# Kernel tuning notes

Measured on AMD Instinct MI355X. Metric: run time of the kernel, lower is better.

## Reference

```python
import jax, jax.numpy as jnp
import numpy as np

LAMBDA_TV = 0.01
RHO = 1.0
MAX_ITER = 10
CG_ITER = 10


def _fft2c(x):
    # x: (B, 2, H, W) real/imag stacked -> centered ortho FFT, same layout
    xc = x[:, 0] + 1j * x[:, 1]
    kc = jnp.fft.fftshift(
        jnp.fft.fft2(jnp.fft.ifftshift(xc, axes=(-2, -1)), norm='ortho'),
        axes=(-2, -1))
    return jnp.stack([kc.real, kc.imag], axis=1)


def _ifft2c(x):
    xc = x[:, 0] + 1j * x[:, 1]
    ic = jnp.fft.fftshift(
        jnp.fft.ifft2(jnp.fft.ifftshift(xc, axes=(-2, -1)), norm='ortho'),
        axes=(-2, -1))
    return jnp.stack([ic.real, ic.imag], axis=1)


def _gradient(x):
    # forward differences, zero at the far boundary; cat along channel dim
    dx = jnp.concatenate([x[..., 1:] - x[..., :-1], jnp.zeros_like(x[..., :1])], axis=-1)
    dy = jnp.concatenate([x[..., 1:, :] - x[..., :-1, :], jnp.zeros_like(x[..., :1, :])], axis=-2)
    return jnp.concatenate([dx, dy], axis=1)


def _divergence(p):
    # Faithful to the original: only uses channels 0 and 1 of p -> (B,1,H,W)
    px, py = p[:, 0:1], p[:, 1:2]
    div_x = jnp.concatenate(
        [px[..., 0:1], px[..., 1:-1] - px[..., :-2], -px[..., -2:-1]], axis=-1)
    div_y = jnp.concatenate(
        [py[..., 0:1, :], py[..., 1:-1, :] - py[..., :-2, :], -py[..., -2:-1, :]], axis=-2)
    return div_x + div_y


def soft_threshold(x, t):
    return jnp.sign(x) * jnp.maximum(jnp.abs(x) - t, 0.0)


def _cg_solve(x0, b, mask):
    # Solves (F^H M F + rho * D^H D) x = b with early-stop semantics of the original
    def A(z):
        return _ifft2c(mask * _fft2c(z)) - RHO * _divergence(_gradient(z))

    r0 = b - A(x0)
    rsold0 = jnp.sum(r0 * r0)

    def step(carry, _):
        x, r, p, rsold, done = carry
        Ap = A(p)
        alpha = rsold / (jnp.sum(p * Ap) + 1e-12)
        xn = x + alpha * p
        rn = r - alpha * Ap
        rsnew = jnp.sum(rn * rn)
        stop = rsnew < 1e-10
        pn = rn + (rsnew / rsold) * p
        x = jnp.where(done, x, xn)
        r = jnp.where(done, r, rn)
        p = jnp.where(done | stop, p, pn)
        rsold = jnp.where(done | stop, rsold, rsnew)
        done = done | stop
        return (x, r, p, rsold, done), None

    init = (x0, r0, r0, rsold0, jnp.array(False))
    (x, _, _, _, _), _ = jax.lax.scan(step, init, None, length=CG_ITER)
    return x


def reference(y, mask):
    x0 = _ifft2c(y)
    u0 = _gradient(x0)
    v0 = jnp.zeros_like(u0)
    b_data = _ifft2c(mask * y)  # constant across outer iterations
    thresh = LAMBDA_TV / RHO

    def step(carry, _):
        x, u, v, done, count, pres_l, dres_l = carry
        b = b_data + RHO * _divergence(u - v)
        xn = _cg_solve(x, b, mask)
        g = _gradient(xn)
        un = soft_threshold(g + v, thresh)
        vn = v + g - un
        pres = jnp.linalg.norm(g - un)
        dres = jnp.linalg.norm(RHO * _divergence(un - u))
        stop = (pres < 1e-4) & (dres < 1e-4)
        x = jnp.where(done, x, xn)
        u = jnp.where(done, u, un)
        v = jnp.where(done, v, vn)
        pres_l = jnp.where(done, pres_l, pres)
        dres_l = jnp.where(done, dres_l, dres)
        count = count + (1 - done.astype(jnp.int32))
        done = done | stop
        return (x, u, v, done, count, pres_l, dres_l), None

    init = (x0, u0, v0, jnp.array(False), jnp.array(0, jnp.int32),
            jnp.array(0.0, x0.dtype), jnp.array(0.0, x0.dtype))
    (x, _, _, _, count, pres, dres), _ = jax.lax.scan(step, init, None, length=MAX_ITER)
    return x, count, pres, dres


def setup_inputs() -> dict:
    key = jax.random.key(0)
    k1, k2 = jax.random.split(key)
    B, H, W = 4, 320, 320
    y = jax.random.normal(k1, (B, 2, H, W), dtype=jnp.float32)
    mask = (jax.random.uniform(k2, (B, 1, H, W)) < 0.3).astype(jnp.float32)
    return {"y": y, "mask": mask}
```

## Files before the change

kernel.cpp:

```cpp
#include <hip/hip_runtime.h>
#include <math.h>

#define DEVFN __device__ __forceinline__

namespace {

constexpr int NW = 320, NH = 320, NHW = NW * NH, NB = 4;
constexpr int NC2 = 2 * NHW;
constexpr int GRID = NB * NH;
constexpr int NTHR = 320;
constexpr float THRESHc = 0.01f;

struct C2 { float x, y; };
DEVFN C2 cmul(C2 a, C2 b) { return C2{a.x * b.x - a.y * b.y, a.x * b.y + a.y * b.x}; }

template <int SIGN>
DEVFN C2 TW(const float2* tw, int m) {
  float2 t = tw[m];
  return C2{t.x, (SIGN < 0) ? t.y : -t.y};
}

DEVFN int swzcol(int bid) { return (bid & 7) * (GRID / 8) + (bid >> 3); }

template <int SIGN, bool MASKED>
__device__ void fftp(float2* A, float2* B, const float2* tw, int t,
                     const float* __restrict__ misRow) {
  const int q = t >> 6, n1 = t & 63;
  __syncthreads();
  C2 acc;
  {
    float2 v0 = A[n1];
    acc.x = v0.x; acc.y = v0.y;
#pragma unroll
    for (int n2 = 1; n2 < 5; n2++) {
      float2 v = A[n1 + 64 * n2];
      C2 w = TW<SIGN>(tw, 64 * ((n2 * q) % 5));
      acc.x += v.x * w.x - v.y * w.y;
      acc.y += v.x * w.y + v.y * w.x;
    }
    acc = cmul(acc, TW<SIGN>(tw, n1 * q));
  }
  B[t] = make_float2(acc.x, acc.y);
  __syncthreads();
  {
    C2 s{0.f, 0.f};
    int rr = n1 & 3, base = (q << 6) + (n1 >> 2);
#pragma unroll
    for (int p = 0; p < 4; p++) {
      float2 v = B[base + 16 * p];
      C2 w = TW<SIGN>(tw, 80 * ((p * rr) & 3));
      s.x += v.x * w.x - v.y * w.y;
      s.y += v.x * w.y + v.y * w.x;
    }
    acc = s;
  }
  A[t] = make_float2(acc.x, acc.y);
  __syncthreads();
  {
    C2 s{0.f, 0.f};
    int rr = n1 & 15, base = (q << 6) + ((n1 >> 4) << 2) + (n1 & 3);
#pragma unroll
    for (int p = 0; p < 4; p++) {
      float2 v = A[base + 16 * p];
      C2 w = TW<SIGN>(tw, 20 * ((p * rr) & 15));
      s.x += v.x * w.x - v.y * w.y;
      s.y += v.x * w.y + v.y * w.x;
    }
    acc = s;
  }
  B[t] = make_float2(acc.x, acc.y);
  __syncthreads();
  {
    C2 s{0.f, 0.f};
    int base = (q << 6) + (n1 & 15);
#pragma unroll
    for (int p = 0; p < 4; p++) {
      float2 v = B[base + 16 * p];
      C2 w = TW<SIGN>(tw, 5 * ((p * n1) & 63));
      s.x += v.x * w.x - v.y * w.y;
      s.y += v.x * w.y + v.y * w.x;
    }
    acc = s;
  }
  int o = 5 * n1 + q;
  if (MASKED) {
    float m = misRow[o];
    acc.x *= m; acc.y *= m;
  }
  A[o] = make_float2(acc.x, acc.y);
  __syncthreads();
}

DEVFN float Gfunc(const float* __restrict__ z, int b, int h, int w) {
  const float* re = z + b * NC2;
  const float* im = re + NHW;
  int hw = h * NW + w;
  float divx, divy;
  if (w == 0) {
    divx = re[hw + 1] - re[hw];
  } else if (w < NW - 1) {
    divx = (re[hw + 1] - re[hw]) - (re[hw] - re[hw - 1]);
  } else {
    divx = -(re[hw] - re[hw - 1]);
  }
  if (h == 0) {
    divy = (w < NW - 1) ? im[hw + 1] - im[hw] : 0.f;
  } else if (h < NH - 1) {
    float a = (w < NW - 1) ? im[hw + 1] - im[hw] : 0.f;
    float bb = (w < NW - 1) ? im[hw - NW + 1] - im[hw - NW] : 0.f;
    divy = a - bb;
  } else {
    divy = -((w < NW - 1) ? im[hw - NW + 1] - im[hw - NW] : 0.f);
  }
  return divx + divy;
}

DEVFN float divUV(const float* __restrict__ u, const float* __restrict__ v, int b, int h, int w) {
  const float* u0 = u + (b * 4 + 0) * NHW; const float* v0 = v + (b * 4 + 0) * NHW;
  const float* u1 = u + (b * 4 + 1) * NHW; const float* v1 = v + (b * 4 + 1) * NHW;
  int hw = h * NW + w;
  float divx, divy;
  if (w == 0)          divx = u0[hw] - v0[hw];
  else if (w < NW - 1) divx = (u0[hw] - v0[hw]) - (u0[hw - 1] - v0[hw - 1]);
  else                 divx = -(u0[hw - 1] - v0[hw - 1]);
  if (h == 0)          divy = u1[hw] - v1[hw];
  else if (h < NH - 1) divy = (u1[hw] - v1[hw]) - (u1[hw - NW] - v1[hw - NW]);
  else                 divy = -(u1[hw - NW] - v1[hw - NW]);
  return divx + divy;
}

DEVFN double shflxd(double v, int m) {
  union { double d; int i[2]; } a; a.d = v;
  a.i[0] = __shfl_xor(a.i[0], m, 64);
  a.i[1] = __shfl_xor(a.i[1], m, 64);
  return a.d;
}
DEVFN double waveRed(double v) {
#pragma unroll
  for (int m = 32; m; m >>= 1) v += shflxd(v, m);
  return v;
}

__device__ double redParts(const double* __restrict__ part, double* sdot, int t) {
  double v = part[t] + part[t + 320] + part[t + 640] + part[t + 960];
  v = waveRed(v);
  if ((t & 63) == 0) sdot[t >> 6] = v;
  __syncthreads();
  double s = sdot[0] + sdot[1] + sdot[2] + sdot[3] + sdot[4];
  __syncthreads();
  return s;
}

__device__ void blockDot1(double a, double* sdot, int t, double* outp) {
  a = waveRed(a);
  if ((t & 63) == 0) sdot[t >> 6] = a;
  __syncthreads();
  if (t == 0) *outp = sdot[0] + sdot[1] + sdot[2] + sdot[3] + sdot[4];
  __syncthreads();
}

__device__ void blockDot3(double a, double b, double c, double* sdot, int t,
                          double* o0, double* o1, double* o2, int bid) {
  a = waveRed(a); b = waveRed(b); c = waveRed(c);
  int wv = t >> 6;
  if ((t & 63) == 0) { sdot[wv * 3] = a; sdot[wv * 3 + 1] = b; sdot[wv * 3 + 2] = c; }
  __syncthreads();
  if (t == 0) {
    double s0 = 0, s1 = 0, s2 = 0;
#pragma unroll
    for (int w2 = 0; w2 < 5; w2++) { s0 += sdot[w2 * 3]; s1 += sdot[w2 * 3 + 1]; s2 += sdot[w2 * 3 + 2]; }
    o0[bid] = s0; o1[bid] = s1; o2[bid] = s2;
  }
  __syncthreads();
}

#define FFTK_SHARED                                     \
  __shared__ float2 sA[320];                            \
  __shared__ float2 sB[320];                            \
  __shared__ float2 stw[320];                           \
  __shared__ double sdot[16];                           \
  (void)sdot;                                           \
  const int t = threadIdx.x;                            \
  const int bid = blockIdx.x;                           \
  stw[t] = twg[t];


__global__ __launch_bounds__(NTHR) void k_init(const float* __restrict__ mask,
                                               float* __restrict__ misT, float2* __restrict__ tw) {
  int t = threadIdx.x, bid = blockIdx.x;
  if (bid == 0) {
    double ang = -2.0 * 3.14159265358979323846 * (double)t / 320.0;
    tw[t] = make_float2((float)cos(ang), (float)sin(ang));
  }
  int i = bid * NTHR + t;
  int b = i / NHW, hw = i % NHW, h = hw / NW, w = hw % NW;
  int hs = (h + 160) % 320, ws = (w + 160) % 320;
  misT[b * NHW + w * NW + h] = mask[b * NHW + hs * NW + ws] * (1.0f / 102400.0f);
}

__global__ __launch_bounds__(NTHR) void k0a(const float* __restrict__ y, const float* __restrict__ mask,
                                            float2* __restrict__ t1, float2* __restrict__ t2,
                                            const float2* __restrict__ twg) {
  FFTK_SHARED
  const int gb = bid / NH, gl = bid % NH;
  const int rowBase = gb * NC2 + gl * NW;
  float sgn = (t & 1) ? -1.f : 1.f;
  sA[t] = make_float2(sgn * y[rowBase + t], sgn * y[rowBase + NHW + t]);
  fftp<1, false>(sA, sB, stw, t, nullptr);
  {
    float2 v = sA[t];
    t1[gb * NHW + gl * NW + t] = make_float2(sgn * v.x, sgn * v.y);
  }
  float m = mask[gb * NHW + gl * NW + t];
  sA[t] = make_float2(sgn * m * y[rowBase + t], sgn * m * y[rowBase + NHW + t]);
  fftp<1, false>(sA, sB, stw, t, nullptr);
  {
    float2 v = sA[t];
    t2[gb * NHW + gl * NW + t] = make_float2(sgn * v.x, sgn * v.y);
  }
}

__global__ __launch_bounds__(NTHR) void k0b(const float2* __restrict__ t1, const float2* __restrict__ t2,
                                            float* __restrict__ x, float* __restrict__ bdata,
                                            const float2* __restrict__ twg) {
  FFTK_SHARED
  const int wid = swzcol(bid);
  const int gb = wid / NH, gl = wid % NH;
  float sgn = (t & 1) ? -1.f : 1.f;
  {
    float2 v = t1[gb * NHW + t * NW + gl];
    sA[t] = make_float2(sgn * v.x, sgn * v.y);
  }
  fftp<1, false>(sA, sB, stw, t, nullptr);
  {
    float2 v = sA[t];
    float s = sgn * (1.f / 320.f);
    x[gb * NC2 + t * NW + gl] = v.x * s;
    x[gb * NC2 + NHW + t * NW + gl] = v.y * s;
  }
  {
    float2 v = t2[gb * NHW + t * NW + gl];
    sA[t] = make_float2(sgn * v.x, sgn * v.y);
  }
  fftp<1, false>(sA, sB, stw, t, nullptr);
  {
    float2 v = sA[t];
    float s = sgn * (1.f / 320.f);
    bdata[gb * NC2 + t * NW + gl] = v.x * s;
    bdata[gb * NC2 + NHW + t * NW + gl] = v.y * s;
  }
}

__global__ __launch_bounds__(NTHR) void ka0(const float* __restrict__ x, float* __restrict__ xc,
                                            float* __restrict__ u, float* __restrict__ v,
                                            float2* __restrict__ t1, const float2* __restrict__ twg) {
  FFTK_SHARED
  const int gb = bid / NH, gl = bid % NH;
  const int rowBase = gb * NC2 + gl * NW;
  {
    int i = bid * NTHR + t;
    int b = i / NHW, hw = i % NHW, h = hw / NW, w = hw % NW;
    const float* re = x + b * NC2;
    const float* im = re + NHW;
    float g0 = (w < NW - 1) ? re[hw + 1] - re[hw] : 0.f;
    float g1 = (w < NW - 1) ? im[hw + 1] - im[hw] : 0.f;
    float g2 = (h < NH - 1) ? re[hw + NW] - re[hw] : 0.f;
    float g3 = (h < NH - 1) ? im[hw + NW] - im[hw] : 0.f;
    int b4 = b * 4 * NHW;
    u[b4 + hw] = g0;           v[b4 + hw] = 0.f;
    u[b4 + NHW + hw] = g1;     v[b4 + NHW + hw] = 0.f;
    u[b4 + 2 * NHW + hw] = g2; v[b4 + 2 * NHW + hw] = 0.f;
    u[b4 + 3 * NHW + hw] = g3; v[b4 + 3 * NHW + hw] = 0.f;
  }
  float re = x[rowBase + t], im = x[rowBase + NHW + t];
  xc[rowBase + t] = re; xc[rowBase + NHW + t] = im;
  sA[t] = make_float2(re, im);
  fftp<-1, false>(sA, sB, stw, t, nullptr);
  t1[gb * NHW + gl * NW + t] = sA[t];
}

__global__ __launch_bounds__(NTHR) void kb(float2* __restrict__ t1, const float* __restrict__ misT,
                                           const float* __restrict__ un, const float* __restrict__ vn,
                                           float* __restrict__ u, float* __restrict__ v,
                                           const double* __restrict__ pPaPrev, const double* __restrict__ pPbPrev,
                                           double* __restrict__ hist_pres, double* __restrict__ hist_dres,
                                           const float2* __restrict__ twg, int it) {
  FFTK_SHARED
  const int wid = swzcol(bid);
  const int gb = wid / NH, gl = wid % NH;
  if (it > 0) {
    double ppa = redParts(pPaPrev, sdot, t);
    double ppb = redParts(pPbPrev, sdot, t);
    if (bid == 0 && t == 0) { hist_pres[it - 1] = ppa; hist_dres[it - 1] = ppb; }
    bool doneA = false;
    for (int j = 0; j <= it - 2; j++) {
      float pr = sqrtf((float)hist_pres[j]), dr = sqrtf((float)hist_dres[j]);
      doneA |= (pr < 1e-4f && dr < 1e-4f);
    }
    if (!doneA) {
      for (int i = wid * NTHR + t; i < NB * 4 * NHW; i += GRID * NTHR) { u[i] = un[i]; v[i] = vn[i]; }
    }
  }
  sA[t] = t1[gb * NHW + t * NW + gl];
  fftp<-1, true>(sA, sB, stw, t, misT + gb * NHW + gl * NW);
  fftp<1, false>(sA, sB, stw, t, nullptr);
  t1[gb * NHW + t * NW + gl] = sA[t];
}

__global__ __launch_bounds__(NTHR) void kcd(float2* __restrict__ t1, const float* __restrict__ x,
                                            const float* __restrict__ u, const float* __restrict__ v,
                                            const float* __restrict__ bdata, float* __restrict__ r,
                                            float* __restrict__ p, double* __restrict__ pRS,
                                            const float2* __restrict__ twg) {
  FFTK_SHARED
  const int gb = bid / NH, gl = bid % NH;
  const int rowBase = gb * NC2 + gl * NW;
  sA[t] = t1[gb * NHW + gl * NW + t];
  fftp<1, false>(sA, sB, stw, t, nullptr);
  float2 Av = sA[t];
  float G = Gfunc(x, gb, gl, t);
  float Ar = Av.x - G, Ai = Av.y - G;
  float d = divUV(u, v, gb, gl, t);
  float br = bdata[rowBase + t] + d;
  float bi = bdata[rowBase + NHW + t] + d;
  float rr = br - Ar, ri = bi - Ai;
  r[rowBase + t] = rr; r[rowBase + NHW + t] = ri;
  p[rowBase + t] = rr; p[rowBase + NHW + t] = ri;
  double acc = (double)rr * rr + (double)ri * ri;
  blockDot1(acc, sdot, t, &pRS[bid]);
  sA[t] = make_float2(rr, ri);
  fftp<-1, false>(sA, sB, stw, t, nullptr);
  t1[gb * NHW + gl * NW + t] = sA[t];
}

__global__ __launch_bounds__(NTHR) void kd(float* __restrict__ xc, float* __restrict__ r,
                                           float* __restrict__ p, const float* __restrict__ Ap,
                                           float2* __restrict__ t1, const double* __restrict__ pRS,
                                           const double* __restrict__ pD0, const double* __restrict__ pD1,
                                           const double* __restrict__ pD2, double* __restrict__ hist_rs,
                                           const float2* __restrict__ twg, int k) {
  FFTK_SHARED
  const int gb = bid / NH, gl = bid % NH;
  const int rowBase = gb * NC2 + gl * NW;
  double pAp = redParts(pD0, sdot, t);
  double rAp = redParts(pD1, sdot, t);
  double A2  = redParts(pD2, sdot, t);
  double rsold = (k == 1) ? redParts(pRS, sdot, t) : hist_rs[k - 2];
  float alpha = (float)rsold / ((float)pAp + 1e-12f);
  double rsnew = rsold - 2.0 * (double)alpha * rAp + (double)alpha * (double)alpha * A2;
  if (bid == 0 && t == 0) hist_rs[k - 1] = rsnew;
  bool doneIn = false;
  for (int j = 0; j <= k - 2; j++) doneIn |= ((float)hist_rs[j] < 1e-10f);
  bool stop = ((float)rsnew < 1e-10f);
  bool doneP = doneIn || stop;
  float beta = (float)rsnew / (float)rsold;
  float pn2[2];
#pragma unroll
  for (int half = 0; half < 2; half++) {
    int a = rowBase + half * NHW + t;
    float pv = p[a], rv = r[a], av = Ap[a], xv = xc[a];
    float rn = rv, xn = xv;
    if (!doneIn) { xn += alpha * pv; rn -= alpha * av; }
    float pn = doneP ? pv : (rn + beta * pv);
    xc[a] = xn; r[a] = rn; p[a] = pn;
    pn2[half] = pn;
  }
  sA[t] = make_float2(pn2[0], pn2[1]);
  fftp<-1, false>(sA, sB, stw, t, nullptr);
  t1[gb * NHW + gl * NW + t] = sA[t];
}

__global__ __launch_bounds__(NTHR) void ke(float2* __restrict__ t1, const float* __restrict__ misT,
                                           const float2* __restrict__ twg) {
  FFTK_SHARED
  const int wid = swzcol(bid);
  const int gb = wid / NH, gl = wid % NH;
  sA[t] = t1[gb * NHW + t * NW + gl];
  fftp<-1, true>(sA, sB, stw, t, misT + gb * NHW + gl * NW);
  fftp<1, false>(sA, sB, stw, t, nullptr);
  t1[gb * NHW + t * NW + gl] = sA[t];
}

__global__ __launch_bounds__(NTHR) void kf(const float2* __restrict__ t1, const float* __restrict__ p,
                                           const float* __restrict__ r, float* __restrict__ Ap,
                                           double* __restrict__ pD0, double* __restrict__ pD1,
                                           double* __restrict__ pD2, const float2* __restrict__ twg) {
  FFTK_SHARED
  const int gb = bid / NH, gl = bid % NH;
  const int rowBase = gb * NC2 + gl * NW;
  sA[t] = t1[gb * NHW + gl * NW + t];
  fftp<1, false>(sA, sB, stw, t, nullptr);
  float2 Av = sA[t];
  float G = Gfunc(p, gb, gl, t);
  float Ar = Av.x - G, Ai = Av.y - G;
  Ap[rowBase + t] = Ar; Ap[rowBase + NHW + t] = Ai;
  float pr = p[rowBase + t], pi = p[rowBase + NHW + t];
  float rr = r[rowBase + t], ri = r[rowBase + NHW + t];
  double aP = (double)pr * Ar + (double)pi * Ai;
  double aR = (double)rr * Ar + (double)ri * Ai;
  double aA = (double)Ar * Ar + (double)Ai * Ai;
  blockDot3(aP, aR, aA, sdot, t, pD0, pD1, pD2, bid);
}

__global__ __launch_bounds__(NTHR) void kh1(const float* __restrict__ xc, const float* __restrict__ p,
                                            const float* __restrict__ v, float2* __restrict__ t1,
                                            float* __restrict__ un, float* __restrict__ vn,
                                            const double* __restrict__ pD0, const double* __restrict__ hist_rs,
                                            double* __restrict__ pPaCur) {
  __shared__ double sdot[16];
  const int t = threadIdx.x, bid = blockIdx.x;
  double pAp = redParts(pD0, sdot, t);
  double rsold = hist_rs[8];
  float alphaF = (float)rsold / ((float)pAp + 1e-12f);
  bool doneX = false;
  for (int j = 0; j <= 8; j++) doneX |= ((float)hist_rs[j] < 1e-10f);
  int i = bid * NTHR + t;
  int b = i / NHW, hw = i % NHW, h = hw / NW, w = hw % NW;
  int base = b * NC2;
  auto XN = [&](int off) {
    float vv = xc[base + off];
    if (!doneX) vv += alphaF * p[base + off];
    return vv;
  };
  float xre = XN(hw), xim = XN(NHW + hw);
  float g0 = 0, g1 = 0, g2 = 0, g3 = 0;
  if (w < NW - 1) { g0 = XN(hw + 1) - xre; g1 = XN(NHW + hw + 1) - xim; }
  if (h < NH - 1) { g2 = XN(hw + NW) - xre; g3 = XN(NHW + hw + NW) - xim; }
  t1[b * NHW + hw] = make_float2(xre, xim);
  float gs[4] = {g0, g1, g2, g3};
  double acc = 0.0;
#pragma unroll
  for (int ch = 0; ch < 4; ch++) {
    int ui = (b * 4 + ch) * NHW + hw;
    float vv = v[ui];
    float sv = gs[ch] + vv;
    float a2 = fabsf(sv) - THRESHc;
    float uo = (a2 > 0.f) ? copysignf(a2, sv) : 0.f;
    un[ui] = uo;
    vn[ui] = vv + gs[ch] - uo;
    float dd = gs[ch] - uo;
    acc += (double)dd * dd;
  }
  blockDot1(acc, sdot, t, &pPaCur[bid]);
}

__global__ __launch_bounds__(NTHR) void kh2a(float* __restrict__ x, float* __restrict__ xc,
                                             float2* __restrict__ t1, const float* __restrict__ un,
                                             const float* __restrict__ u,
                                             const double* __restrict__ hist_pres,
                                             const double* __restrict__ hist_dres,
                                             double* __restrict__ pPbCur,
                                             const float2* __restrict__ twg, int it) {
  FFTK_SHARED
  const int gb = bid / NH, gl = bid % NH;
  const int rowBase = gb * NC2 + gl * NW;
  bool doneA = false;
  for (int j = 0; j <= it - 1; j++) {
    float pr = sqrtf((float)hist_pres[j]), dr = sqrtf((float)hist_dres[j]);
    doneA |= (pr < 1e-4f && dr < 1e-4f);
  }
  {
    int i = bid * NTHR + t;
    int b = i / NHW, hw = i % NHW, h = hw / NW, w = hw % NW;
    const float* N0 = un + (b * 4 + 0) * NHW; const float* U0 = u + (b * 4 + 0) * NHW;
    const float* N1 = un + (b * 4 + 1) * NHW; const float* U1 = u + (b * 4 + 1) * NHW;
    float divx, divy;
    if (w == 0)          divx = N0[hw] - U0[hw];
    else if (w < NW - 1) divx = (N0[hw] - U0[hw]) - (N0[hw - 1] - U0[hw - 1]);
    else                 divx = -(N0[hw - 1] - U0[hw - 1]);
    if (h == 0)          divy = N1[hw] - U1[hw];
    else if (h < NH - 1) divy = (N1[hw] - U1[hw]) - (N1[hw - NW] - U1[hw - NW]);
    else                 divy = -(N1[hw - NW] - U1[hw - NW]);
    float d = divx + divy;
    double acc = (double)d * d;
    blockDot1(acc, sdot, t, &pPbCur[bid]);
  }
  float2 xn = t1[gb * NHW + gl * NW + t];
  float xfr, xfi;
  if (doneA) { xfr = x[rowBase + t]; xfi = x[rowBase + NHW + t]; }
  else       { xfr = xn.x; xfi = xn.y; }
  x[rowBase + t] = xfr; x[rowBase + NHW + t] = xfi;
  xc[rowBase + t] = xfr; xc[rowBase + NHW + t] = xfi;
  sA[t] = make_float2(xfr, xfi);
  fftp<-1, false>(sA, sB, stw, t, nullptr);
  t1[gb * NHW + gl * NW + t] = sA[t];
}

__global__ __launch_bounds__(NTHR) void k_out(const float* __restrict__ x,
                                              const double* __restrict__ hist_pres,
                                              const double* __restrict__ hist_dres,
                                              const double* __restrict__ pPa9,
                                              const double* __restrict__ pPb9,
                                              float* __restrict__ out) {
  __shared__ double sdot[16];
  const int t = threadIdx.x, bid = blockIdx.x;
  for (int i = bid * NTHR + t; i < NB * NC2; i += GRID * NTHR) out[i] = x[i];
  if (bid == 0) {
    double p9 = redParts(pPa9, sdot, t);
    double d9 = redParts(pPb9, sdot, t);
    if (t == 0) {
      int count = 0; bool done = false; float presO = 0.f, dresO = 0.f;
      for (int it = 0; it < 10; ++it) {
        double hp = (it == 9) ? p9 : hist_pres[it];
        double hd = (it == 9) ? d9 : hist_dres[it];
        if (!done) {
          count++;
          presO = sqrtf((float)hp);
          dresO = sqrtf((float)hd);
          done = (presO < 1e-4f) && (dresO < 1e-4f);
        }
      }
      out[NB * NC2 + 0] = (float)count;
      out[NB * NC2 + 1] = presO;
      out[NB * NC2 + 2] = dresO;
    }
  }
}

}

extern "C" void kernel_launch(void* const* d_in, const int* in_sizes, int n_in,
                              void* d_out, int out_size, void* d_ws, size_t ws_size,
                              hipStream_t stream) {
  (void)in_sizes; (void)n_in; (void)out_size; (void)ws_size;
  const float* y = (const float*)d_in[0];
  const float* mask = (const float*)d_in[1];
  float* out = (float*)d_out;
  float* wsf = (float*)d_ws;

  double* dws = (double*)wsf;
  double* pRS       = dws;
  double* pD0       = dws + 1280;
  double* pD1       = dws + 2560;
  double* pD2       = dws + 3840;
  double* pPa       = dws + 5120;
  double* pPb       = dws + 7680;
  double* hist_rs   = dws + 10240;
  double* hist_pres = dws + 10256;
  double* hist_dres = dws + 10272;

  float* fb = wsf + 20576;
  float2* tw = (float2*)fb; fb += 640;
  float* misT = fb; fb += (size_t)NB * NHW;
  float2* t1 = (float2*)fb; fb += (size_t)2 * NB * NHW;
  float2* t2 = (float2*)fb; fb += (size_t)2 * NB * NHW;
  auto take = [&](size_t n) { float* ptr = fb; fb += n; return ptr; };
  float* x     = take((size_t)NB * NC2);
  float* xc    = take((size_t)NB * NC2);
  float* r     = take((size_t)NB * NC2);
  float* p     = take((size_t)NB * NC2);
  float* Ap    = take((size_t)NB * NC2);
  float* bdata = take((size_t)NB * NC2);
  float* u     = take((size_t)NB * 4 * NHW);
  float* v     = take((size_t)NB * 4 * NHW);
  float* un    = take((size_t)NB * 4 * NHW);
  float* vn    = take((size_t)NB * 4 * NHW);

  k_init<<<GRID, NTHR, 0, stream>>>(mask, misT, tw);
  k0a<<<GRID, NTHR, 0, stream>>>(y, mask, t1, t2, tw);
  k0b<<<GRID, NTHR, 0, stream>>>(t1, t2, x, bdata, tw);
  ka0<<<GRID, NTHR, 0, stream>>>(x, xc, u, v, t1, tw);

  for (int it = 0; it < 10; ++it) {
    int prevPar = (it + 1) & 1;
    int curPar = it & 1;
    kb<<<GRID, NTHR, 0, stream>>>(t1, misT, un, vn, u, v,
                                  pPa + prevPar * 1280, pPb + prevPar * 1280,
                                  hist_pres, hist_dres, tw, it);
    kcd<<<GRID, NTHR, 0, stream>>>(t1, x, u, v, bdata, r, p, pRS, tw);
    ke<<<GRID, NTHR, 0, stream>>>(t1, misT, tw);
    kf<<<GRID, NTHR, 0, stream>>>(t1, p, r, Ap, pD0, pD1, pD2, tw);
    for (int k = 1; k < 10; ++k) {
      kd<<<GRID, NTHR, 0, stream>>>(xc, r, p, Ap, t1, pRS, pD0, pD1, pD2, hist_rs, tw, k);
      ke<<<GRID, NTHR, 0, stream>>>(t1, misT, tw);
      kf<<<GRID, NTHR, 0, stream>>>(t1, p, r, Ap, pD0, pD1, pD2, tw);
    }
    kh1<<<GRID, NTHR, 0, stream>>>(xc, p, v, t1, un, vn, pD0, hist_rs, pPa + curPar * 1280);
    kh2a<<<GRID, NTHR, 0, stream>>>(x, xc, t1, un, u, hist_pres, hist_dres,
                                    pPb + curPar * 1280, tw, it);
  }
  k_out<<<GRID, NTHR, 0, stream>>>(x, hist_pres, hist_dres, pPa + 1280, pPb + 1280, out);
}
```

Baseline: 2.998 ms.

## Use radix-8 FFT stages with padded LDS and interleaved complex buffers

```diff
diff --git a/kernel.cpp b/kernel.cpp
--- a/kernel.cpp
+++ b/kernel.cpp
@@ -23,59 +23,46 @@
 DEVFN int swzcol(int bid) { return (bid & 7) * (GRID / 8) + (bid >> 3); }
 
 template <int SIGN, bool MASKED>
-__device__ void fftp(float2* A, float2* B, const float2* tw, int t,
+__device__ void fftp(float2* IN, float2* OUT, const float2* tw, int t,
                      const float* __restrict__ misRow) {
   const int q = t >> 6, n1 = t & 63;
+  const int b72 = q * 72;
   __syncthreads();
   C2 acc;
   {
-    float2 v0 = A[n1];
+    float2 v0 = IN[n1];
     acc.x = v0.x; acc.y = v0.y;
 #pragma unroll
     for (int n2 = 1; n2 < 5; n2++) {
-      float2 v = A[n1 + 64 * n2];
+      float2 v = IN[n1 + 64 * n2];
       C2 w = TW<SIGN>(tw, 64 * ((n2 * q) % 5));
       acc.x += v.x * w.x - v.y * w.y;
       acc.y += v.x * w.y + v.y * w.x;
     }
     acc = cmul(acc, TW<SIGN>(tw, n1 * q));
   }
-  B[t] = make_float2(acc.x, acc.y);
+  OUT[b72 + n1] = make_float2(acc.x, acc.y);
   __syncthreads();
   {
     C2 s{0.f, 0.f};
-    int rr = n1 & 3, base = (q << 6) + (n1 >> 2);
+    const int nlow = n1 & 7, mlow = n1 >> 3;
+    const int base = b72 + nlow;
 #pragma unroll
-    for (int p = 0; p < 4; p++) {
-      float2 v = B[base + 16 * p];
-      C2 w = TW<SIGN>(tw, 80 * ((p * rr) & 3));
+    for (int nh = 0; nh < 8; nh++) {
+      float2 v = OUT[base + 8 * nh];
+      C2 w = TW<SIGN>(tw, 40 * ((nh * mlow) & 7));
       s.x += v.x * w.x - v.y * w.y;
       s.y += v.x * w.y + v.y * w.x;
     }
-    acc = s;
-  }
-  A[t] = make_float2(acc.x, acc.y);
+    IN[b72 + 9 * mlow + nlow] = make_float2(s.x, s.y);
+  }
   __syncthreads();
   {
     C2 s{0.f, 0.f};
-    int rr = n1 & 15, base = (q << 6) + ((n1 >> 4) << 2) + (n1 & 3);
+    const int base = b72 + 9 * (n1 & 7);
 #pragma unroll
-    for (int p = 0; p < 4; p++) {
-      float2 v = A[base + 16 * p];
-      C2 w = TW<SIGN>(tw, 20 * ((p * rr) & 15));
-      s.x += v.x * w.x - v.y * w.y;
-      s.y += v.x * w.y + v.y * w.x;
-    }
-    acc = s;
-  }
-  B[t] = make_float2(acc.x, acc.y);
-  __syncthreads();
-  {
-    C2 s{0.f, 0.f};
-    int base = (q << 6) + (n1 & 15);
-#pragma unroll
-    for (int p = 0; p < 4; p++) {
-      float2 v = B[base + 16 * p];
+    for (int p = 0; p < 8; p++) {
+      float2 v = IN[base + p];
       C2 w = TW<SIGN>(tw, 5 * ((p * n1) & 63));
       s.x += v.x * w.x - v.y * w.y;
       s.y += v.x * w.y + v.y * w.x;
@@ -87,30 +74,29 @@
     float m = misRow[o];
     acc.x *= m; acc.y *= m;
   }
-  A[o] = make_float2(acc.x, acc.y);
-  __syncthreads();
-}
-
-DEVFN float Gfunc(const float* __restrict__ z, int b, int h, int w) {
-  const float* re = z + b * NC2;
-  const float* im = re + NHW;
+  OUT[o] = make_float2(acc.x, acc.y);
+  __syncthreads();
+}
+
+DEVFN float Gfunc2(const float2* __restrict__ z, int b, int h, int w) {
+  const float2* zz = z + b * NHW;
   int hw = h * NW + w;
   float divx, divy;
   if (w == 0) {
-    divx = re[hw + 1] - re[hw];
+    divx = zz[hw + 1].x - zz[hw].x;
   } else if (w < NW - 1) {
-    divx = (re[hw + 1] - re[hw]) - (re[hw] - re[hw - 1]);
+    divx = (zz[hw + 1].x - zz[hw].x) - (zz[hw].x - zz[hw - 1].x);
   } else {
-    divx = -(re[hw] - re[hw - 1]);
+    divx = -(zz[hw].x - zz[hw - 1].x);
   }
   if (h == 0) {
-    divy = (w < NW - 1) ? im[hw + 1] - im[hw] : 0.f;
+    divy = (w < NW - 1) ? zz[hw + 1].y - zz[hw].y : 0.f;
   } else if (h < NH - 1) {
-    float a = (w < NW - 1) ? im[hw + 1] - im[hw] : 0.f;
-    float bb = (w < NW - 1) ? im[hw - NW + 1] - im[hw - NW] : 0.f;
+    float a = (w < NW - 1) ? zz[hw + 1].y - zz[hw].y : 0.f;
+    float bb = (w < NW - 1) ? zz[hw - NW + 1].y - zz[hw - NW].y : 0.f;
     divy = a - bb;
   } else {
-    divy = -((w < NW - 1) ? im[hw - NW + 1] - im[hw - NW] : 0.f);
+    divy = -((w < NW - 1) ? zz[hw - NW + 1].y - zz[hw - NW].y : 0.f);
   }
   return divx + divy;
 }
@@ -175,8 +161,8 @@
 }
 
 #define FFTK_SHARED                                     \
-  __shared__ float2 sA[320];                            \
-  __shared__ float2 sB[320];                            \
+  __shared__ float2 sA[384];                            \
+  __shared__ float2 sB[384];                            \
   __shared__ float2 stw[320];                           \
   __shared__ double sdot[16];                           \
   (void)sdot;                                           \
@@ -208,20 +194,20 @@
   sA[t] = make_float2(sgn * y[rowBase + t], sgn * y[rowBase + NHW + t]);
   fftp<1, false>(sA, sB, stw, t, nullptr);
   {
-    float2 v = sA[t];
+    float2 v = sB[t];
     t1[gb * NHW + gl * NW + t] = make_float2(sgn * v.x, sgn * v.y);
   }
   float m = mask[gb * NHW + gl * NW + t];
   sA[t] = make_float2(sgn * m * y[rowBase + t], sgn * m * y[rowBase + NHW + t]);
   fftp<1, false>(sA, sB, stw, t, nullptr);
   {
-    float2 v = sA[t];
+    float2 v = sB[t];
     t2[gb * NHW + gl * NW + t] = make_float2(sgn * v.x, sgn * v.y);
   }
 }
 
 __global__ __launch_bounds__(NTHR) void k0b(const float2* __restrict__ t1, const float2* __restrict__ t2,
-                                            float* __restrict__ x, float* __restrict__ bdata,
+                                            float2* __restrict__ x2, float2* __restrict__ bdata2,
                                             const float2* __restrict__ twg) {
   FFTK_SHARED
   const int wid = swzcol(bid);
@@ -233,10 +219,9 @@
   }
   fftp<1, false>(sA, sB, stw, t, nullptr);
   {
-    float2 v = sA[t];
+    float2 v = sB[t];
     float s = sgn * (1.f / 320.f);
-    x[gb * NC2 + t * NW + gl] = v.x * s;
-    x[gb * NC2 + NHW + t * NW + gl] = v.y * s;
+    x2[gb * NHW + t * NW + gl] = make_float2(v.x * s, v.y * s);
   }
   {
     float2 v = t2[gb * NHW + t * NW + gl];
@@ -244,39 +229,37 @@
   }
   fftp<1, false>(sA, sB, stw, t, nullptr);
   {
-    float2 v = sA[t];
+    float2 v = sB[t];
     float s = sgn * (1.f / 320.f);
-    bdata[gb * NC2 + t * NW + gl] = v.x * s;
-    bdata[gb * NC2 + NHW + t * NW + gl] = v.y * s;
-  }
-}
-
-__global__ __launch_bounds__(NTHR) void ka0(const float* __restrict__ x, float* __restrict__ xc,
+    bdata2[gb * NHW + t * NW + gl] = make_float2(v.x * s, v.y * s);
+  }
+}
+
+__global__ __launch_bounds__(NTHR) void ka0(const float2* __restrict__ x2, float2* __restrict__ xc2,
                                             float* __restrict__ u, float* __restrict__ v,
                                             float2* __restrict__ t1, const float2* __restrict__ twg) {
   FFTK_SHARED
   const int gb = bid / NH, gl = bid % NH;
-  const int rowBase = gb * NC2 + gl * NW;
   {
     int i = bid * NTHR + t;
     int b = i / NHW, hw = i % NHW, h = hw / NW, w = hw % NW;
-    const float* re = x + b * NC2;
-    const float* im = re + NHW;
-    float g0 = (w < NW - 1) ? re[hw + 1] - re[hw] : 0.f;
-    float g1 = (w < NW - 1) ? im[hw + 1] - im[hw] : 0.f;
-    float g2 = (h < NH - 1) ? re[hw + NW] - re[hw] : 0.f;
-    float g3 = (h < NH - 1) ? im[hw + NW] - im[hw] : 0.f;
+    const float2* zz = x2 + b * NHW;
+    float2 z0 = zz[hw];
+    float g0 = 0, g1 = 0, g2 = 0, g3 = 0;
+    if (w < NW - 1) { float2 zr = zz[hw + 1]; g0 = zr.x - z0.x; g1 = zr.y - z0.y; }
+    if (h < NH - 1) { float2 zd = zz[hw + NW]; g2 = zd.x - z0.x; g3 = zd.y - z0.y; }
     int b4 = b * 4 * NHW;
     u[b4 + hw] = g0;           v[b4 + hw] = 0.f;
     u[b4 + NHW + hw] = g1;     v[b4 + NHW + hw] = 0.f;
     u[b4 + 2 * NHW + hw] = g2; v[b4 + 2 * NHW + hw] = 0.f;
     u[b4 + 3 * NHW + hw] = g3; v[b4 + 3 * NHW + hw] = 0.f;
   }
-  float re = x[rowBase + t], im = x[rowBase + NHW + t];
-  xc[rowBase + t] = re; xc[rowBase + NHW + t] = im;
-  sA[t] = make_float2(re, im);
+  int idx = gb * NHW + gl * NW + t;
+  float2 xv = x2[idx];
+  xc2[idx] = xv;
+  sA[t] = xv;
   fftp<-1, false>(sA, sB, stw, t, nullptr);
-  t1[gb * NHW + gl * NW + t] = sA[t];
+  t1[idx] = sB[t];
 }
 
 __global__ __launch_bounds__(NTHR) void kb(float2* __restrict__ t1, const float* __restrict__ misT,
@@ -303,45 +286,44 @@
   }
   sA[t] = t1[gb * NHW + t * NW + gl];
   fftp<-1, true>(sA, sB, stw, t, misT + gb * NHW + gl * NW);
+  fftp<1, false>(sB, sA, stw, t, nullptr);
+  t1[gb * NHW + t * NW + gl] = sA[t];
+}
+
+__global__ __launch_bounds__(NTHR) void kcd(float2* __restrict__ t1, const float2* __restrict__ x2,
+                                            const float* __restrict__ u, const float* __restrict__ v,
+                                            const float2* __restrict__ bdata2, float2* __restrict__ r2,
+                                            float2* __restrict__ p2, double* __restrict__ pRS,
+                                            const float2* __restrict__ twg) {
+  FFTK_SHARED
+  const int gb = bid / NH, gl = bid % NH;
+  const int idx = gb * NHW + gl * NW + t;
+  sA[t] = t1[idx];
   fftp<1, false>(sA, sB, stw, t, nullptr);
-  t1[gb * NHW + t * NW + gl] = sA[t];
-}
-
-__global__ __launch_bounds__(NTHR) void kcd(float2* __restrict__ t1, const float* __restrict__ x,
-                                            const float* __restrict__ u, const float* __restrict__ v,
-                                            const float* __restrict__ bdata, float* __restrict__ r,
-                                            float* __restrict__ p, double* __restrict__ pRS,
-                                            const float2* __restrict__ twg) {
-  FFTK_SHARED
-  const int gb = bid / NH, gl = bid % NH;
-  const int rowBase = gb * NC2 + gl * NW;
-  sA[t] = t1[gb * NHW + gl * NW + t];
-  fftp<1, false>(sA, sB, stw, t, nullptr);
-  float2 Av = sA[t];
-  float G = Gfunc(x, gb, gl, t);
-  float Ar = Av.x - G, Ai = Av.y - G;
+  float2 Av = sB[t];
+  float G = Gfunc2(x2, gb, gl, t);
   float d = divUV(u, v, gb, gl, t);
-  float br = bdata[rowBase + t] + d;
-  float bi = bdata[rowBase + NHW + t] + d;
-  float rr = br - Ar, ri = bi - Ai;
-  r[rowBase + t] = rr; r[rowBase + NHW + t] = ri;
-  p[rowBase + t] = rr; p[rowBase + NHW + t] = ri;
+  float2 bd = bdata2[idx];
+  float rr = (bd.x + d) - (Av.x - G);
+  float ri = (bd.y + d) - (Av.y - G);
+  float2 rv = make_float2(rr, ri);
+  r2[idx] = rv; p2[idx] = rv;
   double acc = (double)rr * rr + (double)ri * ri;
   blockDot1(acc, sdot, t, &pRS[bid]);
-  sA[t] = make_float2(rr, ri);
+  sA[t] = rv;
   fftp<-1, false>(sA, sB, stw, t, nullptr);
-  t1[gb * NHW + gl * NW + t] = sA[t];
-}
-
-__global__ __launch_bounds__(NTHR) void kd(float* __restrict__ xc, float* __restrict__ r,
-                                           float* __restrict__ p, const float* __restrict__ Ap,
+  t1[idx] = sB[t];
+}
+
+__global__ __launch_bounds__(NTHR) void kd(float2* __restrict__ xc2, float2* __restrict__ r2,
+                                           float2* __restrict__ p2, const float2* __restrict__ Ap2,
                                            float2* __restrict__ t1, const double* __restrict__ pRS,
                                            const double* __restrict__ pD0, const double* __restrict__ pD1,
                                            const double* __restrict__ pD2, double* __restrict__ hist_rs,
                                            const float2* __restrict__ twg, int k) {
   FFTK_SHARED
   const int gb = bid / NH, gl = bid % NH;
-  const int rowBase = gb * NC2 + gl * NW;
+  const int idx = gb * NHW + gl * NW + t;
   double pAp = redParts(pD0, sdot, t);
   double rAp = redParts(pD1, sdot, t);
   double A2  = redParts(pD2, sdot, t);
@@ -354,20 +336,16 @@
   bool stop = ((float)rsnew < 1e-10f);
   bool doneP = doneIn || stop;
   float beta = (float)rsnew / (float)rsold;
-  float pn2[2];
-#pragma unroll
-  for (int half = 0; half < 2; half++) {
-    int a = rowBase + half * NHW + t;
-    float pv = p[a], rv = r[a], av = Ap[a], xv = xc[a];
-    float rn = rv, xn = xv;
-    if (!doneIn) { xn += alpha * pv; rn -= alpha * av; }
-    float pn = doneP ? pv : (rn + beta * pv);
-    xc[a] = xn; r[a] = rn; p[a] = pn;
-    pn2[half] = pn;
-  }
-  sA[t] = make_float2(pn2[0], pn2[1]);
+  float2 pv = p2[idx], rv = r2[idx], av = Ap2[idx], xv = xc2[idx];
+  if (!doneIn) {
+    xv.x += alpha * pv.x; xv.y += alpha * pv.y;
+    rv.x -= alpha * av.x; rv.y -= alpha * av.y;
+  }
+  float2 pn = doneP ? pv : make_float2(rv.x + beta * pv.x, rv.y + beta * pv.y);
+  xc2[idx] = xv; r2[idx] = rv; p2[idx] = pn;
+  sA[t] = pn;
   fftp<-1, false>(sA, sB, stw, t, nullptr);
-  t1[gb * NHW + gl * NW + t] = sA[t];
+  t1[idx] = sB[t];
 }
 
 __global__ __launch_bounds__(NTHR) void ke(float2* __restrict__ t1, const float* __restrict__ misT,
@@ -377,32 +355,31 @@
   const int gb = wid / NH, gl = wid % NH;
   sA[t] = t1[gb * NHW + t * NW + gl];
   fftp<-1, true>(sA, sB, stw, t, misT + gb * NHW + gl * NW);
-  fftp<1, false>(sA, sB, stw, t, nullptr);
+  fftp<1, false>(sB, sA, stw, t, nullptr);
   t1[gb * NHW + t * NW + gl] = sA[t];
 }
 
-__global__ __launch_bounds__(NTHR) void kf(const float2* __restrict__ t1, const float* __restrict__ p,
-                                           const float* __restrict__ r, float* __restrict__ Ap,
+__global__ __launch_bounds__(NTHR) void kf(const float2* __restrict__ t1, const float2* __restrict__ p2,
+                                           const float2* __restrict__ r2, float2* __restrict__ Ap2,
                                            double* __restrict__ pD0, double* __restrict__ pD1,
                                            double* __restrict__ pD2, const float2* __restrict__ twg) {
   FFTK_SHARED
   const int gb = bid / NH, gl = bid % NH;
-  const int rowBase = gb * NC2 + gl * NW;
-  sA[t] = t1[gb * NHW + gl * NW + t];
+  const int idx = gb * NHW + gl * NW + t;
+  sA[t] = t1[idx];
   fftp<1, false>(sA, sB, stw, t, nullptr);
-  float2 Av = sA[t];
-  float G = Gfunc(p, gb, gl, t);
+  float2 Av = sB[t];
+  float G = Gfunc2(p2, gb, gl, t);
   float Ar = Av.x - G, Ai = Av.y - G;
-  Ap[rowBase + t] = Ar; Ap[rowBase + NHW + t] = Ai;
-  float pr = p[rowBase + t], pi = p[rowBase + NHW + t];
-  float rr = r[rowBase + t], ri = r[rowBase + NHW + t];
-  double aP = (double)pr * Ar + (double)pi * Ai;
-  double aR = (double)rr * Ar + (double)ri * Ai;
+  Ap2[idx] = make_float2(Ar, Ai);
+  float2 pv = p2[idx], rv = r2[idx];
+  double aP = (double)pv.x * Ar + (double)pv.y * Ai;
+  double aR = (double)rv.x * Ar + (double)rv.y * Ai;
   double aA = (double)Ar * Ar + (double)Ai * Ai;
   blockDot3(aP, aR, aA, sdot, t, pD0, pD1, pD2, bid);
 }
 
-__global__ __launch_bounds__(NTHR) void kh1(const float* __restrict__ xc, const float* __restrict__ p,
+__global__ __launch_bounds__(NTHR) void kh1(const float2* __restrict__ xc2, const float2* __restrict__ p2,
                                             const float* __restrict__ v, float2* __restrict__ t1,
                                             float* __restrict__ un, float* __restrict__ vn,
                                             const double* __restrict__ pD0, const double* __restrict__ hist_rs,
@@ -416,17 +393,20 @@
   for (int j = 0; j <= 8; j++) doneX |= ((float)hist_rs[j] < 1e-10f);
   int i = bid * NTHR + t;
   int b = i / NHW, hw = i % NHW, h = hw / NW, w = hw % NW;
-  int base = b * NC2;
+  int base2 = b * NHW;
   auto XN = [&](int off) {
-    float vv = xc[base + off];
-    if (!doneX) vv += alphaF * p[base + off];
+    float2 vv = xc2[base2 + off];
+    if (!doneX) {
+      float2 pp = p2[base2 + off];
+      vv.x += alphaF * pp.x; vv.y += alphaF * pp.y;
+    }
     return vv;
   };
-  float xre = XN(hw), xim = XN(NHW + hw);
+  float2 x0 = XN(hw);
   float g0 = 0, g1 = 0, g2 = 0, g3 = 0;
-  if (w < NW - 1) { g0 = XN(hw + 1) - xre; g1 = XN(NHW + hw + 1) - xim; }
-  if (h < NH - 1) { g2 = XN(hw + NW) - xre; g3 = XN(NHW + hw + NW) - xim; }
-  t1[b * NHW + hw] = make_float2(xre, xim);
+  if (w < NW - 1) { float2 xr = XN(hw + 1); g0 = xr.x - x0.x; g1 = xr.y - x0.y; }
+  if (h < NH - 1) { float2 xd = XN(hw + NW); g2 = xd.x - x0.x; g3 = xd.y - x0.y; }
+  t1[base2 + hw] = x0;
   float gs[4] = {g0, g1, g2, g3};
   double acc = 0.0;
 #pragma unroll
@@ -444,7 +424,7 @@
   blockDot1(acc, sdot, t, &pPaCur[bid]);
 }
 
-__global__ __launch_bounds__(NTHR) void kh2a(float* __restrict__ x, float* __restrict__ xc,
+__global__ __launch_bounds__(NTHR) void kh2a(float2* __restrict__ x2, float2* __restrict__ xc2,
                                              float2* __restrict__ t1, const float* __restrict__ un,
                                              const float* __restrict__ u,
                                              const double* __restrict__ hist_pres,
@@ -453,7 +433,7 @@
                                              const float2* __restrict__ twg, int it) {
   FFTK_SHARED
   const int gb = bid / NH, gl = bid % NH;
-  const int rowBase = gb * NC2 + gl * NW;
+  const int idx = gb * NHW + gl * NW + t;
   bool doneA = false;
   for (int j = 0; j <= it - 1; j++) {
     float pr = sqrtf((float)hist_pres[j]), dr = sqrtf((float)hist_dres[j]);
@@ -475,18 +455,15 @@
     double acc = (double)d * d;
     blockDot1(acc, sdot, t, &pPbCur[bid]);
   }
-  float2 xn = t1[gb * NHW + gl * NW + t];
-  float xfr, xfi;
-  if (doneA) { xfr = x[rowBase + t]; xfi = x[rowBase + NHW + t]; }
-  else       { xfr = xn.x; xfi = xn.y; }
-  x[rowBase + t] = xfr; x[rowBase + NHW + t] = xfi;
-  xc[rowBase + t] = xfr; xc[rowBase + NHW + t] = xfi;
-  sA[t] = make_float2(xfr, xfi);
+  float2 xn = t1[idx];
+  float2 xf = doneA ? x2[idx] : xn;
+  x2[idx] = xf; xc2[idx] = xf;
+  sA[t] = xf;
   fftp<-1, false>(sA, sB, stw, t, nullptr);
-  t1[gb * NHW + gl * NW + t] = sA[t];
-}
-
-__global__ __launch_bounds__(NTHR) void k_out(const float* __restrict__ x,
+  t1[idx] = sB[t];
+}
+
+__global__ __launch_bounds__(NTHR) void k_out(const float2* __restrict__ x2,
                                               const double* __restrict__ hist_pres,
                                               const double* __restrict__ hist_dres,
                                               const double* __restrict__ pPa9,
@@ -494,7 +471,13 @@
                                               float* __restrict__ out) {
   __shared__ double sdot[16];
   const int t = threadIdx.x, bid = blockIdx.x;
-  for (int i = bid * NTHR + t; i < NB * NC2; i += GRID * NTHR) out[i] = x[i];
+  {
+    int i = bid * NTHR + t;
+    int b = i / NHW, hw = i % NHW;
+    float2 v = x2[b * NHW + hw];
+    out[b * NC2 + hw] = v.x;
+    out[b * NC2 + NHW + hw] = v.y;
+  }
   if (bid == 0) {
     double p9 = redParts(pPa9, sdot, t);
     double d9 = redParts(pPb9, sdot, t);
@@ -544,22 +527,23 @@
   float* misT = fb; fb += (size_t)NB * NHW;
   float2* t1 = (float2*)fb; fb += (size_t)2 * NB * NHW;
   float2* t2 = (float2*)fb; fb += (size_t)2 * NB * NHW;
+  auto take2 = [&](size_t n) { float2* ptr = (float2*)fb; fb += 2 * n; return ptr; };
+  float2* x2     = take2((size_t)NB * NHW);
+  float2* xc2    = take2((size_t)NB * NHW);
+  float2* r2     = take2((size_t)NB * NHW);
+  float2* p2     = take2((size_t)NB * NHW);
+  float2* Ap2    = take2((size_t)NB * NHW);
+  float2* bdata2 = take2((size_t)NB * NHW);
   auto take = [&](size_t n) { float* ptr = fb; fb += n; return ptr; };
-  float* x     = take((size_t)NB * NC2);
-  float* xc    = take((size_t)NB * NC2);
-  float* r     = take((size_t)NB * NC2);
-  float* p     = take((size_t)NB * NC2);
-  float* Ap    = take((size_t)NB * NC2);
-  float* bdata = take((size_t)NB * NC2);
-  float* u     = take((size_t)NB * 4 * NHW);
-  float* v     = take((size_t)NB * 4 * NHW);
-  float* un    = take((size_t)NB * 4 * NHW);
-  float* vn    = take((size_t)NB * 4 * NHW);
+  float* u  = take((size_t)NB * 4 * NHW);
+  float* v  = take((size_t)NB * 4 * NHW);
+  float* un = take((size_t)NB * 4 * NHW);
+  float* vn = take((size_t)NB * 4 * NHW);
 
   k_init<<<GRID, NTHR, 0, stream>>>(mask, misT, tw);
   k0a<<<GRID, NTHR, 0, stream>>>(y, mask, t1, t2, tw);
-  k0b<<<GRID, NTHR, 0, stream>>>(t1, t2, x, bdata, tw);
-  ka0<<<GRID, NTHR, 0, stream>>>(x, xc, u, v, t1, tw);
+  k0b<<<GRID, NTHR, 0, stream>>>(t1, t2, x2, bdata2, tw);
+  ka0<<<GRID, NTHR, 0, stream>>>(x2, xc2, u, v, t1, tw);
 
   for (int it = 0; it < 10; ++it) {
     int prevPar = (it + 1) & 1;
@@ -567,17 +551,17 @@
     kb<<<GRID, NTHR, 0, stream>>>(t1, misT, un, vn, u, v,
                                   pPa + prevPar * 1280, pPb + prevPar * 1280,
                                   hist_pres, hist_dres, tw, it);
-    kcd<<<GRID, NTHR, 0, stream>>>(t1, x, u, v, bdata, r, p, pRS, tw);
+    kcd<<<GRID, NTHR, 0, stream>>>(t1, x2, u, v, bdata2, r2, p2, pRS, tw);
     ke<<<GRID, NTHR, 0, stream>>>(t1, misT, tw);
-    kf<<<GRID, NTHR, 0, stream>>>(t1, p, r, Ap, pD0, pD1, pD2, tw);
+    kf<<<GRID, NTHR, 0, stream>>>(t1, p2, r2, Ap2, pD0, pD1, pD2, tw);
     for (int k = 1; k < 10; ++k) {
-      kd<<<GRID, NTHR, 0, stream>>>(xc, r, p, Ap, t1, pRS, pD0, pD1, pD2, hist_rs, tw, k);
+      kd<<<GRID, NTHR, 0, stream>>>(xc2, r2, p2, Ap2, t1, pRS, pD0, pD1, pD2, hist_rs, tw, k);
       ke<<<GRID, NTHR, 0, stream>>>(t1, misT, tw);
-      kf<<<GRID, NTHR, 0, stream>>>(t1, p, r, Ap, pD0, pD1, pD2, tw);
-    }
-    kh1<<<GRID, NTHR, 0, stream>>>(xc, p, v, t1, un, vn, pD0, hist_rs, pPa + curPar * 1280);
-    kh2a<<<GRID, NTHR, 0, stream>>>(x, xc, t1, un, u, hist_pres, hist_dres,
+      kf<<<GRID, NTHR, 0, stream>>>(t1, p2, r2, Ap2, pD0, pD1, pD2, tw);
+    }
+    kh1<<<GRID, NTHR, 0, stream>>>(xc2, p2, v, t1, un, vn, pD0, hist_rs, pPa + curPar * 1280);
+    kh2a<<<GRID, NTHR, 0, stream>>>(x2, xc2, t1, un, u, hist_pres, hist_dres,
                                     pPb + curPar * 1280, tw, it);
   }
-  k_out<<<GRID, NTHR, 0, stream>>>(x, hist_pres, hist_dres, pPa + 1280, pPb + 1280, out);
-}
+  k_out<<<GRID, NTHR, 0, stream>>>(x2, hist_pres, hist_dres, pPa + 1280, pPb + 1280, out);
+}
```

After: 3.140 ms. +4.8%, slower.
